# Kernel optimization log

Measured on AMD Instinct MI355X. Metric: run time of the kernel, lower is better.

## Reference

```python
import jax, jax.numpy as jnp
import numpy as np

EPS = 1e-5


def setup_inputs() -> dict:
    key = jax.random.key(0)
    ks = jax.random.split(key, 6)
    B, C, H, W = 32, 256, 32, 32
    T, O, K, KS = 256, 256, 4, 3
    return {
        "x": jax.random.normal(ks[0], (B, C, H, W), dtype=jnp.float32),
        "z": jax.random.normal(ks[1], (B, T), dtype=jnp.float32),
        "w1": jax.random.normal(ks[2], (T, T + C), dtype=jnp.float32) * 0.05,
        "bn_gamma": jnp.ones((T,), jnp.float32),
        "bn_beta": jnp.zeros((T,), jnp.float32),
        "bn_mean": jnp.zeros((T,), jnp.float32),
        "bn_var": jnp.ones((T,), jnp.float32),
        "w2": jax.random.normal(ks[3], (K, T), dtype=jnp.float32) * 0.05,
        "weight": jax.random.normal(ks[4], (K, O, C, KS, KS), dtype=jnp.float32) * 0.05,
        "static_weight": jax.random.normal(ks[5], (O, C, KS, KS), dtype=jnp.float32) * 0.05,
    }


def _kernel_attention(x, z, w1, bn_gamma, bn_beta, bn_mean, bn_var, w2):
    # x: [B,C,H,W], z: [B,T] -> att: [B,K]
    avg = jnp.mean(x, axis=(2, 3))                 # adaptive avg pool to 1x1 -> [B,C]
    a = jnp.concatenate([z, avg], axis=1)          # [B, T+C]
    h = a @ w1.T                                   # 1x1 conv on 1x1 spatial == matmul
    h = (h - bn_mean) / jnp.sqrt(bn_var + EPS) * bn_gamma + bn_beta  # BN (eval)
    h = jax.nn.relu(h)
    att = h @ w2.T                                 # [B,K]
    return jax.nn.sigmoid(att)                     # temperature = 1.0


def reference(x, z, w1, bn_gamma, bn_beta, bn_mean, bn_var, w2, weight, static_weight):
    B = x.shape[0]
    att = _kernel_attention(x, z, w1, bn_gamma, bn_beta, bn_mean, bn_var, w2)  # [B,K]
    # per-sample mixed weights: [B,O,C,k,k]
    agg_w = jnp.einsum('bk,koihw->boihw', att, weight * 0.1) + static_weight[None]

    def conv_one(xi, wi):
        # xi: [C,H,W], wi: [O,C,k,k]
        out = jax.lax.conv_general_dilated(
            xi[None], wi, window_strides=(1, 1), padding=[(1, 1), (1, 1)],
            dimension_numbers=('NCHW', 'OIHW', 'NCHW'))
        return out[0]

    return jax.vmap(conv_one)(x, agg_w)            # [B,O,H,W]
```

## Files before the change

kernel.cpp:

```cpp
#include <hip/hip_runtime.h>
#include <hip/hip_bf16.h>

typedef __attribute__((ext_vector_type(4))) float f32x4;
typedef __attribute__((ext_vector_type(8))) short bf16x8;
typedef __attribute__((ext_vector_type(8))) unsigned short ushort8;

#define EPSBN 1e-5f

__device__ __forceinline__ unsigned short f2bf(float f) {
  unsigned int u = __builtin_bit_cast(unsigned int, f);
  u += 0x7fffu + ((u >> 16) & 1u);
  return (unsigned short)(u >> 16);
}

__device__ __forceinline__ void gload_lds16(const unsigned short* g, unsigned short* l) {
  __builtin_amdgcn_global_load_lds(
      (const __attribute__((address_space(1))) void*)g,
      (__attribute__((address_space(3))) void*)l, 16, 0, 0);
}

__global__ __launch_bounds__(256) void prep_kernel(const float* __restrict__ x,
                                                   float* __restrict__ avg,
                                                   unsigned short* __restrict__ xpad) {
  int blk = blockIdx.x;
  int b = blk >> 5, cg = blk & 31;
  int t = threadIdx.x;
  int c = t >> 5, l32 = t & 31;
  __shared__ unsigned short lds_t[1024 * 9];
  __shared__ float avg_lds[8];
  const float4* xb4 = reinterpret_cast<const float4*>(x) + ((size_t)(b * 256 + cg * 8 + c)) * 256;
  float s = 0.f;
#pragma unroll
  for (int i = 0; i < 8; ++i) {
    float4 v = xb4[l32 + 32 * i];
    s += v.x + v.y + v.z + v.w;
    int p = 4 * (l32 + 32 * i);
    lds_t[(p + 0) * 9 + c] = f2bf(v.x);
    lds_t[(p + 1) * 9 + c] = f2bf(v.y);
    lds_t[(p + 2) * 9 + c] = f2bf(v.z);
    lds_t[(p + 3) * 9 + c] = f2bf(v.w);
  }
#pragma unroll
  for (int off = 16; off >= 1; off >>= 1) s += __shfl_down(s, off, 32);
  if (l32 == 0) avg_lds[c] = s;
  __syncthreads();
  if (t < 8) avg[b * 256 + cg * 8 + t] = avg_lds[t] * (1.0f / 1024.0f);
  size_t obase = (size_t)blk * 1156 * 8;
  for (int sIdx = t; sIdx < 1156; sIdx += 256) {
    int h = sIdx / 34, w = sIdx % 34;
    ushort8 v;
    if (h >= 1 && h <= 32 && w >= 1 && w <= 32) {
      int p = (h - 1) * 32 + (w - 1);
#pragma unroll
      for (int cl = 0; cl < 8; ++cl) v[cl] = lds_t[p * 9 + cl];
    } else {
#pragma unroll
      for (int cl = 0; cl < 8; ++cl) v[cl] = 0;
    }
    *reinterpret_cast<ushort8*>(xpad + obase + (size_t)sIdx * 8) = v;
  }
}

__global__ __launch_bounds__(256) void att_kernel(
    const float* __restrict__ z, const float* __restrict__ avg,
    const float* __restrict__ w1, const float* __restrict__ gamma,
    const float* __restrict__ beta, const float* __restrict__ mean,
    const float* __restrict__ var, const float* __restrict__ w2,
    float* __restrict__ att) {
  int b = blockIdx.x, t = threadIdx.x;
  __shared__ __align__(16) float a[512];
  __shared__ float h[256];
  a[t] = z[b * 256 + t];
  a[t + 256] = avg[b * 256 + t];
  __syncthreads();
  const float4* wr = reinterpret_cast<const float4*>(w1 + (size_t)t * 512);
  const float4* a4 = reinterpret_cast<const float4*>(a);
  float s = 0.f;
#pragma unroll 4
  for (int j = 0; j < 128; ++j) {
    float4 wv = wr[j], av = a4[j];
    s += wv.x * av.x + wv.y * av.y + wv.z * av.z + wv.w * av.w;
  }
  s = (s - mean[t]) * rsqrtf(var[t] + EPSBN) * gamma[t] + beta[t];
  h[t] = fmaxf(s, 0.f);
  __syncthreads();
  int wv_ = t >> 6, lane = t & 63;
  const float* w2r = w2 + wv_ * 256;
  float p = h[lane] * w2r[lane] + h[lane + 64] * w2r[lane + 64] +
            h[lane + 128] * w2r[lane + 128] + h[lane + 192] * w2r[lane + 192];
#pragma unroll
  for (int off = 32; off >= 1; off >>= 1) p += __shfl_down(p, off);
  if (lane == 0) att[b * 4 + wv_] = 1.0f / (1.0f + expf(-p));
}

#define MROW 291
__global__ __launch_bounds__(256) void mix_kernel(
    const float* __restrict__ weight, const float* __restrict__ statw,
    const float* __restrict__ att, unsigned short* __restrict__ agg) {
  int cc = blockIdx.x >> 5;
  int og = blockIdx.x & 31;
  int o0 = og * 8;
  int t = threadIdx.x;
  __shared__ float ldsf[5][8][MROW];
  __shared__ float att_lds[128];
  if (t < 128) att_lds[t] = att[t];
  const float* bases[5] = {statw, weight, weight + 589824, weight + 2 * 589824,
                           weight + 3 * 589824};
#pragma unroll
  for (int i = 0; i < 12; ++i) {
    int L = i * 256 + t;
    if (L < 2880) {
      int a = L / 576;
      int r = L % 576;
      int o_l = r / 72;
      int q = r % 72;
      float4 v = *reinterpret_cast<const float4*>(bases[a] + (size_t)(o0 + o_l) * 2304 +
                                                  cc * 288 + q * 4);
      float* d = &ldsf[a][o_l][q * 4];
      d[0] = v.x; d[1] = v.y; d[2] = v.z; d[3] = v.w;
    }
  }
  __syncthreads();
  for (int slot = t; slot < 288; slot += 256) {
    int o_l = slot & 7;
    int cblk = (slot >> 3) & 3;
    int tap = slot >> 5;
    float sv[8], wk0[8], wk1[8], wk2[8], wk3[8];
#pragma unroll
    for (int cl = 0; cl < 8; ++cl) {
      int idx9 = (cblk * 8 + cl) * 9 + tap;
      sv[cl] = ldsf[0][o_l][idx9];
      wk0[cl] = ldsf[1][o_l][idx9];
      wk1[cl] = ldsf[2][o_l][idx9];
      wk2[cl] = ldsf[3][o_l][idx9];
      wk3[cl] = ldsf[4][o_l][idx9];
    }
    size_t obase = ((size_t)(tap * 8 + cc) * 4 + cblk) * 256 + (o0 + o_l);
    for (int b = 0; b < 32; ++b) {
      float a0 = 0.1f * att_lds[b * 4 + 0];
      float a1 = 0.1f * att_lds[b * 4 + 1];
      float a2 = 0.1f * att_lds[b * 4 + 2];
      float a3 = 0.1f * att_lds[b * 4 + 3];
      ushort8 outv;
#pragma unroll
      for (int cl = 0; cl < 8; ++cl) {
        float v = sv[cl] + a0 * wk0[cl] + a1 * wk1[cl] + a2 * wk2[cl] + a3 * wk3[cl];
        outv[cl] = f2bf(v);
      }
      *reinterpret_cast<ushort8*>(agg + ((size_t)b * 73728 + obase) * 8) = outv;
    }
  }
}

__global__ __launch_bounds__(256, 2) void conv_kernel(
    const unsigned short* __restrict__ xpad, const unsigned short* __restrict__ agg,
    float* __restrict__ out) {
  int wgid = (blockIdx.x & 7) * 64 + (blockIdx.x >> 3);
  int pt = wgid & 7;
  int ot = (wgid >> 3) & 1;
  int b = wgid >> 4;
  int h0 = pt * 4;

  __shared__ __align__(16) unsigned short x_lds[2][8192];

  int tid = threadIdx.x;
  int lane = tid & 63, wv = tid >> 6;
  int wave_mo = (wv & 1) * 64;
  int wave_no = (wv >> 1) * 64;
  int kb = lane >> 4, ln = lane & 15;

  f32x4 acc[4][4];
#pragma unroll
  for (int i = 0; i < 4; ++i)
#pragma unroll
    for (int j = 0; j < 4; ++j) acc[i][j] = (f32x4){0.f, 0.f, 0.f, 0.f};

  const unsigned short* aggL =
      agg + (size_t)b * 589824 + ((size_t)kb * 256 + ot * 128 + wave_mo + ln) * 8;

  auto issueX = [&](int cc, int bsel) {
    const unsigned short* g = xpad + ((size_t)(b * 32 + cc * 4 + wv) * 1156 + h0 * 34) * 8;
    unsigned short* l = &x_lds[bsel][wv * 2048];
#pragma unroll
    for (int i = 0; i < 4; ++i) gload_lds16(g + i * 512 + lane * 8, l + i * 512);
  };

  issueX(0, 0);
  __syncthreads();

  bf16x8 af[4];
#pragma unroll 1
  for (int cc = 0; cc < 8; ++cc) {
    if (cc < 7) issueX(cc + 1, (cc + 1) & 1);
    const unsigned short* aggC = aggL + (size_t)(0 * 8 + cc) * 8192;
#pragma unroll
    for (int ai = 0; ai < 4; ++ai)
      af[ai] = *reinterpret_cast<const bf16x8*>(aggC + (size_t)ai * 128);
    const unsigned short* xb = &x_lds[cc & 1][kb * 2048];
#pragma unroll
    for (int tap = 0; tap < 9; ++tap) {
      bf16x8 afn[4];
      if (tap < 8) {
        const unsigned short* aggN = aggL + (size_t)((tap + 1) * 8 + cc) * 8192;
#pragma unroll
        for (int ai = 0; ai < 4; ++ai)
          afn[ai] = *reinterpret_cast<const bf16x8*>(aggN + (size_t)ai * 128);
      }
      int dh = tap / 3, dw = tap % 3;
      bf16x8 bfr[4];
#pragma unroll
      for (int bj = 0; bj < 4; ++bj) {
        int p = wave_no + bj * 16 + ln;
        int rr = (p >> 5) + dh;
        int wc = (p & 31) + dw;
        bfr[bj] = *reinterpret_cast<const bf16x8*>(xb + (rr * 34 + wc) * 8);
      }
      __builtin_amdgcn_s_setprio(1);
#pragma unroll
      for (int ai = 0; ai < 4; ++ai)
#pragma unroll
        for (int bj = 0; bj < 4; ++bj)
          acc[ai][bj] =
              __builtin_amdgcn_mfma_f32_16x16x32_bf16(af[ai], bfr[bj], acc[ai][bj], 0, 0, 0);
      __builtin_amdgcn_s_setprio(0);
      if (tap < 8) {
#pragma unroll
        for (int ai = 0; ai < 4; ++ai) af[ai] = afn[ai];
      }
    }
    __syncthreads();
  }

  size_t ob = ((size_t)b * 256 + ot * 128 + wave_mo) * 1024 + (size_t)pt * 128 + wave_no;
#pragma unroll
  for (int ai = 0; ai < 4; ++ai)
#pragma unroll
    for (int bj = 0; bj < 4; ++bj) {
#pragma unroll
      for (int v = 0; v < 4; ++v) {
        int oo = ai * 16 + (lane >> 4) * 4 + v;
        out[ob + (size_t)oo * 1024 + bj * 16 + ln] = acc[ai][bj][v];
      }
    }
}

extern "C" void kernel_launch(void* const* d_in, const int* in_sizes, int n_in,
                              void* d_out, int out_size, void* d_ws, size_t ws_size,
                              hipStream_t stream) {
  const float* x = (const float*)d_in[0];
  const float* z = (const float*)d_in[1];
  const float* w1 = (const float*)d_in[2];
  const float* gamma = (const float*)d_in[3];
  const float* beta = (const float*)d_in[4];
  const float* mean = (const float*)d_in[5];
  const float* var = (const float*)d_in[6];
  const float* w2 = (const float*)d_in[7];
  const float* weight = (const float*)d_in[8];
  const float* statw = (const float*)d_in[9];
  float* out = (float*)d_out;

  float* att = (float*)d_ws;
  float* avg = (float*)((char*)d_ws + 1024);
  unsigned short* xpad = (unsigned short*)((char*)d_ws + 65536);
  unsigned short* agg = (unsigned short*)((char*)d_ws + 19009536);

  prep_kernel<<<1024, 256, 0, stream>>>(x, avg, xpad);
  att_kernel<<<32, 256, 0, stream>>>(z, avg, w1, gamma, beta, mean, var, w2, att);
  mix_kernel<<<256, 256, 0, stream>>>(weight, statw, att, agg);
  conv_kernel<<<512, 256, 0, stream>>>(xpad, agg, out);
}
```

Measured before the change: 83.86 us.

## Halve conv output tile per block, raise occupancy, deepen weight prefetch

Each conv workgroup now covers 64 output channels instead of 128, so the grid doubles to 1024 blocks. Launch bounds go from 2 to 4 blocks per SIMD/CU target, giving more waves to hide latency. The per-sample weight fragments are prefetched two taps ahead through a rotating register pipeline, and the next x tile load is issued later, at tap 7. In exchange, each xpad tile is now loaded by twice as many blocks, and there is less MFMA work per LDS read of the B fragments.

```diff
diff --git a/kernel.cpp b/kernel.cpp
--- a/kernel.cpp
+++ b/kernel.cpp
@@ -152,31 +152,32 @@
   }
 }
 
-__global__ __launch_bounds__(256, 2) void conv_kernel(
+__global__ __launch_bounds__(256, 4) void conv_kernel(
     const unsigned short* __restrict__ xpad, const unsigned short* __restrict__ agg,
     float* __restrict__ out) {
-  int wgid = (blockIdx.x & 7) * 64 + (blockIdx.x >> 3);
-  int pt = wgid & 7;
-  int ot = (wgid >> 3) & 1;
-  int b = wgid >> 4;
+  int wgid = (blockIdx.x & 7) * 128 + (blockIdx.x >> 3);
+  int b = wgid >> 5;
+  int r = wgid & 31;
+  int ot = r >> 3;
+  int pt = r & 7;
   int h0 = pt * 4;
 
-  __shared__ __align__(16) unsigned short x_lds[2][8192];
+  __shared__ __align__(16) unsigned short x_lds[2][4 * 2048];
 
   int tid = threadIdx.x;
   int lane = tid & 63, wv = tid >> 6;
-  int wave_mo = (wv & 1) * 64;
+  int wave_mo = (wv & 1) * 32;
   int wave_no = (wv >> 1) * 64;
   int kb = lane >> 4, ln = lane & 15;
 
-  f32x4 acc[4][4];
-#pragma unroll
-  for (int i = 0; i < 4; ++i)
+  f32x4 acc[2][4];
+#pragma unroll
+  for (int i = 0; i < 2; ++i)
 #pragma unroll
     for (int j = 0; j < 4; ++j) acc[i][j] = (f32x4){0.f, 0.f, 0.f, 0.f};
 
   const unsigned short* aggL =
-      agg + (size_t)b * 589824 + ((size_t)kb * 256 + ot * 128 + wave_mo + ln) * 8;
+      agg + (size_t)b * 589824 + ((size_t)kb * 256 + ot * 64 + wave_mo + ln) * 8;
 
   auto issueX = [&](int cc, int bsel) {
     const unsigned short* g = xpad + ((size_t)(b * 32 + cc * 4 + wv) * 1156 + h0 * 34) * 8;
@@ -184,28 +185,29 @@
 #pragma unroll
     for (int i = 0; i < 4; ++i) gload_lds16(g + i * 512 + lane * 8, l + i * 512);
   };
+  auto loadA = [&](int tg, bf16x8* dst) {
+    const unsigned short* g = aggL + (size_t)tg * 8192;
+    dst[0] = *reinterpret_cast<const bf16x8*>(g);
+    dst[1] = *reinterpret_cast<const bf16x8*>(g + 128);
+  };
 
   issueX(0, 0);
-  __syncthreads();
-
-  bf16x8 af[4];
+  bf16x8 A0[2], A1[2], A2[2];
+  loadA(0 * 8 + 0, A0);
+  loadA(1 * 8 + 0, A1);
+  __syncthreads();
+
 #pragma unroll 1
   for (int cc = 0; cc < 8; ++cc) {
-    if (cc < 7) issueX(cc + 1, (cc + 1) & 1);
-    const unsigned short* aggC = aggL + (size_t)(0 * 8 + cc) * 8192;
-#pragma unroll
-    for (int ai = 0; ai < 4; ++ai)
-      af[ai] = *reinterpret_cast<const bf16x8*>(aggC + (size_t)ai * 128);
     const unsigned short* xb = &x_lds[cc & 1][kb * 2048];
 #pragma unroll
     for (int tap = 0; tap < 9; ++tap) {
-      bf16x8 afn[4];
-      if (tap < 8) {
-        const unsigned short* aggN = aggL + (size_t)((tap + 1) * 8 + cc) * 8192;
-#pragma unroll
-        for (int ai = 0; ai < 4; ++ai)
-          afn[ai] = *reinterpret_cast<const bf16x8*>(aggN + (size_t)ai * 128);
-      }
+      if (tap < 7) {
+        loadA((tap + 2) * 8 + cc, A2);
+      } else if (cc < 7) {
+        loadA((tap - 7) * 8 + (cc + 1), A2);
+      }
+      if (tap == 7 && cc < 7) issueX(cc + 1, (cc + 1) & 1);
       int dh = tap / 3, dw = tap % 3;
       bf16x8 bfr[4];
 #pragma unroll
@@ -217,23 +219,24 @@
       }
       __builtin_amdgcn_s_setprio(1);
 #pragma unroll
-      for (int ai = 0; ai < 4; ++ai)
+      for (int ai = 0; ai < 2; ++ai)
 #pragma unroll
         for (int bj = 0; bj < 4; ++bj)
           acc[ai][bj] =
-              __builtin_amdgcn_mfma_f32_16x16x32_bf16(af[ai], bfr[bj], acc[ai][bj], 0, 0, 0);
+              __builtin_amdgcn_mfma_f32_16x16x32_bf16(A0[ai], bfr[bj], acc[ai][bj], 0, 0, 0);
       __builtin_amdgcn_s_setprio(0);
-      if (tap < 8) {
-#pragma unroll
-        for (int ai = 0; ai < 4; ++ai) af[ai] = afn[ai];
+#pragma unroll
+      for (int ai = 0; ai < 2; ++ai) {
+        A0[ai] = A1[ai];
+        A1[ai] = A2[ai];
       }
     }
     __syncthreads();
   }
 
-  size_t ob = ((size_t)b * 256 + ot * 128 + wave_mo) * 1024 + (size_t)pt * 128 + wave_no;
-#pragma unroll
-  for (int ai = 0; ai < 4; ++ai)
+  size_t ob = ((size_t)b * 256 + ot * 64 + wave_mo) * 1024 + (size_t)pt * 128 + wave_no;
+#pragma unroll
+  for (int ai = 0; ai < 2; ++ai)
 #pragma unroll
     for (int bj = 0; bj < 4; ++bj) {
 #pragma unroll
@@ -267,5 +270,5 @@
   prep_kernel<<<1024, 256, 0, stream>>>(x, avg, xpad);
   att_kernel<<<32, 256, 0, stream>>>(z, avg, w1, gamma, beta, mean, var, w2, att);
   mix_kernel<<<256, 256, 0, stream>>>(weight, statw, att, agg);
-  conv_kernel<<<512, 256, 0, stream>>>(xpad, agg, out);
-}
+  conv_kernel<<<1024, 256, 0, stream>>>(xpad, agg, out);
+}
```

After: 86.68 us. 1.03x slower.

## Switch conv inner loop to 32x32x16 bf16 MFMA tiles

Applied to the files above, without the earlier changes.

Replaces the 16x16x32 MFMA tiling (4x4 accumulators per wave) with 32x32x16 MFMAs (2x2 accumulators of 16 floats), remapping the A-fragment loads from the aggregated weights and the B-fragment reads from the padded input in LDS. Larger MFMA tiles issue fewer instructions and fewer LDS reads per FLOP. The next-chunk input prefetch now starts late in the tap loop instead of at the top of the iteration, and the setprio hints are dropped. The output store index mapping changes to match the 32x32 accumulator layout.

```diff
diff --git a/kernel.cpp b/kernel.cpp
--- a/kernel.cpp
+++ b/kernel.cpp
@@ -2,6 +2,7 @@
 #include <hip/hip_bf16.h>
 
 typedef __attribute__((ext_vector_type(4))) float f32x4;
+typedef __attribute__((ext_vector_type(16))) float f32x16;
 typedef __attribute__((ext_vector_type(8))) short bf16x8;
 typedef __attribute__((ext_vector_type(8))) unsigned short ushort8;
 
@@ -161,22 +162,32 @@
   int b = wgid >> 4;
   int h0 = pt * 4;
 
-  __shared__ __align__(16) unsigned short x_lds[2][8192];
+  __shared__ __align__(16) unsigned short x_lds[2][4 * 2048];
 
   int tid = threadIdx.x;
   int lane = tid & 63, wv = tid >> 6;
   int wave_mo = (wv & 1) * 64;
   int wave_no = (wv >> 1) * 64;
-  int kb = lane >> 4, ln = lane & 15;
-
-  f32x4 acc[4][4];
-#pragma unroll
-  for (int i = 0; i < 4; ++i)
-#pragma unroll
-    for (int j = 0; j < 4; ++j) acc[i][j] = (f32x4){0.f, 0.f, 0.f, 0.f};
+  int l31 = lane & 31, kh = lane >> 5;
+
+  f32x16 acc[2][2];
+#pragma unroll
+  for (int i = 0; i < 2; ++i)
+#pragma unroll
+    for (int j = 0; j < 2; ++j)
+#pragma unroll
+      for (int e = 0; e < 16; ++e) acc[i][j][e] = 0.f;
 
   const unsigned short* aggL =
-      agg + (size_t)b * 589824 + ((size_t)kb * 256 + ot * 128 + wave_mo + ln) * 8;
+      agg + (size_t)b * 589824 + ((size_t)kh * 256 + ot * 128 + wave_mo + l31) * 8;
+  auto loadA = [&](int tg, bf16x8* dst) {
+    const unsigned short* g = aggL + (size_t)tg * 8192;
+#pragma unroll
+    for (int ks = 0; ks < 2; ++ks)
+#pragma unroll
+      for (int m = 0; m < 2; ++m)
+        dst[ks * 2 + m] = *reinterpret_cast<const bf16x8*>(g + ks * 4096 + m * 256);
+  };
 
   auto issueX = [&](int cc, int bsel) {
     const unsigned short* g = xpad + ((size_t)(b * 32 + cc * 4 + wv) * 1156 + h0 * 34) * 8;
@@ -188,58 +199,50 @@
   issueX(0, 0);
   __syncthreads();
 
-  bf16x8 af[4];
+  int rbase = wave_no >> 5;
 #pragma unroll 1
   for (int cc = 0; cc < 8; ++cc) {
-    if (cc < 7) issueX(cc + 1, (cc + 1) & 1);
-    const unsigned short* aggC = aggL + (size_t)(0 * 8 + cc) * 8192;
-#pragma unroll
-    for (int ai = 0; ai < 4; ++ai)
-      af[ai] = *reinterpret_cast<const bf16x8*>(aggC + (size_t)ai * 128);
-    const unsigned short* xb = &x_lds[cc & 1][kb * 2048];
+    const unsigned short* xb0 = &x_lds[cc & 1][0];
+    bf16x8 af[4];
+    loadA(cc, af);
 #pragma unroll
     for (int tap = 0; tap < 9; ++tap) {
       bf16x8 afn[4];
       if (tap < 8) {
-        const unsigned short* aggN = aggL + (size_t)((tap + 1) * 8 + cc) * 8192;
-#pragma unroll
-        for (int ai = 0; ai < 4; ++ai)
-          afn[ai] = *reinterpret_cast<const bf16x8*>(aggN + (size_t)ai * 128);
+        loadA((tap + 1) * 8 + cc, afn);
       }
+      if (tap == 7 && cc < 7) issueX(cc + 1, (cc + 1) & 1);
       int dh = tap / 3, dw = tap % 3;
-      bf16x8 bfr[4];
-#pragma unroll
-      for (int bj = 0; bj < 4; ++bj) {
-        int p = wave_no + bj * 16 + ln;
-        int rr = (p >> 5) + dh;
-        int wc = (p & 31) + dw;
-        bfr[bj] = *reinterpret_cast<const bf16x8*>(xb + (rr * 34 + wc) * 8);
-      }
-      __builtin_amdgcn_s_setprio(1);
-#pragma unroll
-      for (int ai = 0; ai < 4; ++ai)
-#pragma unroll
-        for (int bj = 0; bj < 4; ++bj)
-          acc[ai][bj] =
-              __builtin_amdgcn_mfma_f32_16x16x32_bf16(af[ai], bfr[bj], acc[ai][bj], 0, 0, 0);
-      __builtin_amdgcn_s_setprio(0);
-      if (tap < 8) {
-#pragma unroll
-        for (int ai = 0; ai < 4; ++ai) af[ai] = afn[ai];
-      }
+      bf16x8 bfr[2][2];
+#pragma unroll
+      for (int ks = 0; ks < 2; ++ks)
+#pragma unroll
+        for (int n = 0; n < 2; ++n)
+          bfr[ks][n] = *reinterpret_cast<const bf16x8*>(
+              xb0 + (2 * ks + kh) * 2048 + ((rbase + n + dh) * 34 + l31 + dw) * 8);
+#pragma unroll
+      for (int ks = 0; ks < 2; ++ks)
+#pragma unroll
+        for (int m = 0; m < 2; ++m)
+#pragma unroll
+          for (int n = 0; n < 2; ++n)
+            acc[m][n] = __builtin_amdgcn_mfma_f32_32x32x16_bf16(af[ks * 2 + m], bfr[ks][n],
+                                                                acc[m][n], 0, 0, 0);
+#pragma unroll
+      for (int i = 0; i < 4; ++i) af[i] = afn[i];
     }
     __syncthreads();
   }
 
   size_t ob = ((size_t)b * 256 + ot * 128 + wave_mo) * 1024 + (size_t)pt * 128 + wave_no;
 #pragma unroll
-  for (int ai = 0; ai < 4; ++ai)
-#pragma unroll
-    for (int bj = 0; bj < 4; ++bj) {
-#pragma unroll
-      for (int v = 0; v < 4; ++v) {
-        int oo = ai * 16 + (lane >> 4) * 4 + v;
-        out[ob + (size_t)oo * 1024 + bj * 16 + ln] = acc[ai][bj][v];
+  for (int m = 0; m < 2; ++m)
+#pragma unroll
+    for (int n = 0; n < 2; ++n) {
+#pragma unroll
+      for (int reg = 0; reg < 16; ++reg) {
+        int oo = m * 32 + (reg & 3) + 8 * (reg >> 2) + 4 * kh;
+        out[ob + (size_t)oo * 1024 + n * 32 + l31] = acc[m][n][reg];
       }
     }
 }
```

Measured after the change: 125.5 us. 49.7% more time.
